# Kernel optimization log

Measured on AMD Instinct MI355X. Metric: run time of the kernel, lower is better.

The kernel has to match this reference:

```python
import jax, jax.numpy as jnp
import numpy as np
from jax import lax

EPS = 1e-06
S = 0.025
ALPHA = 0.98
DELTA = 2.0
R = 0.5


def setup_inputs() -> dict:
    key = jax.random.key(0)
    # magnitude spectrogram: [batch, freq, time], nonnegative
    x = jax.random.uniform(key, (32, 256, 4096), dtype=jnp.float32)
    return {"x": x}


def reference(x):
    # x: [B, F, T]; EMA smoother runs over the time axis (last dim).
    # m_0 = s*x_0 ; m_t = (1-s)*m_{t-1} + s*x_t  (init carry 0 reproduces m_0 = s*x_0)
    xt = jnp.moveaxis(x, 2, 0)  # [T, B, F]

    def step(m, frame):
        m = (1.0 - S) * m + S * frame
        return m, m

    _, M = lax.scan(step, jnp.zeros_like(xt[0]), xt)  # [T, B, F]
    M = jnp.moveaxis(M, 0, 2)  # [B, F, T]
    # power-law compression fused elementwise
    return (x / (M + EPS) ** ALPHA + DELTA) ** R - DELTA ** R
```

## Files before the change

### kernel.cpp

```cpp
#include <hip/hip_runtime.h>


constexpr int T_LEN = 4096;
constexpr int CHUNK = 1024;
constexpr int WARM  = 256;

constexpr float EPSF = 1e-6f;
constexpr float SF   = 0.025f;
constexpr float A1F  = 0.975f;

constexpr double dA1   = 0.975;
constexpr double dA2   = dA1 * dA1;
constexpr double dA4   = dA2 * dA2;
constexpr double dA8   = dA4 * dA4;
constexpr double dA16  = dA8 * dA8;
constexpr double dA32  = dA16 * dA16;
constexpr double dA64  = dA32 * dA32;
constexpr double dA128 = dA64 * dA64;
constexpr double dA256 = dA128 * dA128;
constexpr double dA512 = dA256 * dA256;

__global__ __launch_bounds__(256, 8) void pcen_kernel(
    const float* __restrict__ x, float* __restrict__ out)
{
    const int tid  = threadIdx.x;
    const int lane = tid & 63;
    const int wave = tid >> 6;
    const long long rbase = (long long)blockIdx.x * T_LEN;
    const int cbase = wave * CHUNK;

    const float4* __restrict__ px   = (const float4*)(x + rbase);
    float4* __restrict__       pout = (float4*)(out + rbase);

    const int f0 = (cbase >> 2) + lane * 4;
    float4 v0 = px[f0 + 0];
    float4 v1 = px[f0 + 1];
    float4 v2 = px[f0 + 2];
    float4 v3 = px[f0 + 3];
    float4 wv = make_float4(0.f, 0.f, 0.f, 0.f);
    if (wave > 0)
        wv = px[((cbase - WARM) >> 2) + lane];

    float T = 0.f;
    if (wave > 0) {
        float Lw = SF * wv.x;
        Lw = fmaf(A1F, Lw, SF * wv.y);
        Lw = fmaf(A1F, Lw, SF * wv.z);
        Lw = fmaf(A1F, Lw, SF * wv.w);
        int e = 63 - lane;
        float f = 1.f;
        if (e & 1)  f *= (float)dA4;
        if (e & 2)  f *= (float)dA8;
        if (e & 4)  f *= (float)dA16;
        if (e & 8)  f *= (float)dA32;
        if (e & 16) f *= (float)dA64;
        if (e & 32) f *= (float)dA128;
        float vs = f * Lw;
        vs += __shfl_xor(vs, 1,  64);
        vs += __shfl_xor(vs, 2,  64);
        vs += __shfl_xor(vs, 4,  64);
        vs += __shfl_xor(vs, 8,  64);
        vs += __shfl_xor(vs, 16, 64);
        vs += __shfl_xor(vs, 32, 64);
        T = vs;
    }

    float xv[16] = { v0.x, v0.y, v0.z, v0.w,
                     v1.x, v1.y, v1.z, v1.w,
                     v2.x, v2.y, v2.z, v2.w,
                     v3.x, v3.y, v3.z, v3.w };
    float S = 0.f;
#pragma unroll
    for (int k = 0; k < 16; ++k) S = fmaf(A1F, S, SF * xv[k]);

    float P = S, t;
    t = __shfl_up(P, 1,  64); if (lane >= 1)  P = fmaf((float)dA16,  t, P);
    t = __shfl_up(P, 2,  64); if (lane >= 2)  P = fmaf((float)dA32,  t, P);
    t = __shfl_up(P, 4,  64); if (lane >= 4)  P = fmaf((float)dA64,  t, P);
    t = __shfl_up(P, 8,  64); if (lane >= 8)  P = fmaf((float)dA128, t, P);
    t = __shfl_up(P, 16, 64); if (lane >= 16) P = fmaf((float)dA256, t, P);
    t = __shfl_up(P, 32, 64); if (lane >= 32) P = fmaf((float)dA512, t, P);

    float carry = __shfl_up(P, 1, 64);
    if (lane == 0) carry = 0.f;
    {
        int e = lane;
        float f = 1.f;
        if (e & 1)  f *= (float)dA16;
        if (e & 2)  f *= (float)dA32;
        if (e & 4)  f *= (float)dA64;
        if (e & 8)  f *= (float)dA128;
        if (e & 16) f *= (float)dA256;
        if (e & 32) f *= (float)dA512;
        carry = fmaf(f, T, carry);
    }

    const float SQRT_D = 1.41421356237309515f;
    float m = carry;
#pragma unroll
    for (int g = 0; g < 4; ++g) {
        float4 r;
        float* rp = &r.x;
#pragma unroll
        for (int j = 0; j < 4; ++j) {
            float xx = xv[g * 4 + j];
            m = fmaf(A1F, m, SF * xx);
            float p = __builtin_amdgcn_exp2f(-0.98f * __builtin_amdgcn_logf(m + EPSF));
            rp[j] = __fsqrt_rn(fmaf(xx, p, 2.0f)) - SQRT_D;
        }
        pout[f0 + g] = r;
    }
}

extern "C" void kernel_launch(void* const* d_in, const int* in_sizes, int n_in,
                              void* d_out, int out_size, void* d_ws, size_t ws_size,
                              hipStream_t stream) {
    const float* x = (const float*)d_in[0];
    float* out = (float*)d_out;
    const int rows = in_sizes[0] / T_LEN;
    pcen_kernel<<<dim3(rows), dim3(256), 0, stream>>>(x, out);
}
```

Baseline: 236.6 us.

## Use persistent grid-stride blocks with next-row prefetch and nontemporal stores

Launches a fixed grid of 2048 blocks that loop over the 8192 rows, loading the next row's data into registers while computing the current one. Per-lane decay factors are hoisted out of the loop, and outputs are written with nontemporal stores. The aim is to hide load latency and cut launch/tail overhead in a memory-bound kernel. In exchange it uses more registers, drops the occupancy hint, and runs fewer blocks, which could reduce memory-level parallelism.

```diff
diff --git a/kernel.cpp b/kernel.cpp
--- a/kernel.cpp
+++ b/kernel.cpp
@@ -4,10 +4,13 @@
 constexpr int T_LEN = 4096;
 constexpr int CHUNK = 1024;
 constexpr int WARM  = 256;
+constexpr int NBLK  = 2048;
 
 constexpr float EPSF = 1e-6f;
 constexpr float SF   = 0.025f;
 constexpr float A1F  = 0.975f;
+
+typedef float vfloat4 __attribute__((ext_vector_type(4)));
 
 constexpr double dA1   = 0.975;
 constexpr double dA2   = dA1 * dA1;
@@ -20,95 +23,120 @@
 constexpr double dA256 = dA128 * dA128;
 constexpr double dA512 = dA256 * dA256;
 
-__global__ __launch_bounds__(256, 8) void pcen_kernel(
-    const float* __restrict__ x, float* __restrict__ out)
+__global__ __launch_bounds__(256) void pcen_kernel(
+    const float* __restrict__ x, float* __restrict__ out, int rows)
 {
     const int tid  = threadIdx.x;
     const int lane = tid & 63;
     const int wave = tid >> 6;
-    const long long rbase = (long long)blockIdx.x * T_LEN;
     const int cbase = wave * CHUNK;
+    const int f0 = (cbase >> 2) + lane * 4;
+    const int fw = ((cbase - WARM) >> 2) + lane;
+    const int RQ = T_LEN / 4;
 
-    const float4* __restrict__ px   = (const float4*)(x + rbase);
-    float4* __restrict__       pout = (float4*)(out + rbase);
+    const vfloat4* __restrict__ px = (const vfloat4*)x;
 
-    const int f0 = (cbase >> 2) + lane * 4;
-    float4 v0 = px[f0 + 0];
-    float4 v1 = px[f0 + 1];
-    float4 v2 = px[f0 + 2];
-    float4 v3 = px[f0 + 3];
-    float4 wv = make_float4(0.f, 0.f, 0.f, 0.f);
-    if (wave > 0)
-        wv = px[((cbase - WARM) >> 2) + lane];
-
-    float T = 0.f;
-    if (wave > 0) {
-        float Lw = SF * wv.x;
-        Lw = fmaf(A1F, Lw, SF * wv.y);
-        Lw = fmaf(A1F, Lw, SF * wv.z);
-        Lw = fmaf(A1F, Lw, SF * wv.w);
+    float fwarm = 1.f;
+    {
         int e = 63 - lane;
-        float f = 1.f;
-        if (e & 1)  f *= (float)dA4;
-        if (e & 2)  f *= (float)dA8;
-        if (e & 4)  f *= (float)dA16;
-        if (e & 8)  f *= (float)dA32;
-        if (e & 16) f *= (float)dA64;
-        if (e & 32) f *= (float)dA128;
-        float vs = f * Lw;
-        vs += __shfl_xor(vs, 1,  64);
-        vs += __shfl_xor(vs, 2,  64);
-        vs += __shfl_xor(vs, 4,  64);
-        vs += __shfl_xor(vs, 8,  64);
-        vs += __shfl_xor(vs, 16, 64);
-        vs += __shfl_xor(vs, 32, 64);
-        T = vs;
+        if (e & 1)  fwarm *= (float)dA4;
+        if (e & 2)  fwarm *= (float)dA8;
+        if (e & 4)  fwarm *= (float)dA16;
+        if (e & 8)  fwarm *= (float)dA32;
+        if (e & 16) fwarm *= (float)dA64;
+        if (e & 32) fwarm *= (float)dA128;
+    }
+    float fcarry = 1.f;
+    {
+        int e = lane;
+        if (e & 1)  fcarry *= (float)dA16;
+        if (e & 2)  fcarry *= (float)dA32;
+        if (e & 4)  fcarry *= (float)dA64;
+        if (e & 8)  fcarry *= (float)dA128;
+        if (e & 16) fcarry *= (float)dA256;
+        if (e & 32) fcarry *= (float)dA512;
     }
 
-    float xv[16] = { v0.x, v0.y, v0.z, v0.w,
-                     v1.x, v1.y, v1.z, v1.w,
-                     v2.x, v2.y, v2.z, v2.w,
-                     v3.x, v3.y, v3.z, v3.w };
-    float S = 0.f;
-#pragma unroll
-    for (int k = 0; k < 16; ++k) S = fmaf(A1F, S, SF * xv[k]);
+    const vfloat4 zero4 = {0.f, 0.f, 0.f, 0.f};
 
-    float P = S, t;
-    t = __shfl_up(P, 1,  64); if (lane >= 1)  P = fmaf((float)dA16,  t, P);
-    t = __shfl_up(P, 2,  64); if (lane >= 2)  P = fmaf((float)dA32,  t, P);
-    t = __shfl_up(P, 4,  64); if (lane >= 4)  P = fmaf((float)dA64,  t, P);
-    t = __shfl_up(P, 8,  64); if (lane >= 8)  P = fmaf((float)dA128, t, P);
-    t = __shfl_up(P, 16, 64); if (lane >= 16) P = fmaf((float)dA256, t, P);
-    t = __shfl_up(P, 32, 64); if (lane >= 32) P = fmaf((float)dA512, t, P);
-
-    float carry = __shfl_up(P, 1, 64);
-    if (lane == 0) carry = 0.f;
-    {
-        int e = lane;
-        float f = 1.f;
-        if (e & 1)  f *= (float)dA16;
-        if (e & 2)  f *= (float)dA32;
-        if (e & 4)  f *= (float)dA64;
-        if (e & 8)  f *= (float)dA128;
-        if (e & 16) f *= (float)dA256;
-        if (e & 32) f *= (float)dA512;
-        carry = fmaf(f, T, carry);
+    int r = blockIdx.x;
+    vfloat4 v0 = zero4, v1 = zero4, v2 = zero4, v3 = zero4, wv = zero4;
+    if (r < rows) {
+        long long rb = (long long)r * RQ;
+        v0 = px[rb + f0 + 0];
+        v1 = px[rb + f0 + 1];
+        v2 = px[rb + f0 + 2];
+        v3 = px[rb + f0 + 3];
+        if (wave > 0) wv = px[rb + fw];
     }
 
     const float SQRT_D = 1.41421356237309515f;
-    float m = carry;
+
+    while (r < rows) {
+        const int rn = r + NBLK;
+        vfloat4 n0 = zero4, n1 = zero4, n2 = zero4, n3 = zero4, nw = zero4;
+        if (rn < rows) {
+            long long rbn = (long long)rn * RQ;
+            n0 = px[rbn + f0 + 0];
+            n1 = px[rbn + f0 + 1];
+            n2 = px[rbn + f0 + 2];
+            n3 = px[rbn + f0 + 3];
+            if (wave > 0) nw = px[rbn + fw];
+        }
+
+        float T = 0.f;
+        if (wave > 0) {
+            float Lw = SF * wv.x;
+            Lw = fmaf(A1F, Lw, SF * wv.y);
+            Lw = fmaf(A1F, Lw, SF * wv.z);
+            Lw = fmaf(A1F, Lw, SF * wv.w);
+            float vs = fwarm * Lw;
+            vs += __shfl_xor(vs, 1,  64);
+            vs += __shfl_xor(vs, 2,  64);
+            vs += __shfl_xor(vs, 4,  64);
+            vs += __shfl_xor(vs, 8,  64);
+            vs += __shfl_xor(vs, 16, 64);
+            vs += __shfl_xor(vs, 32, 64);
+            T = vs;
+        }
+
+        float xv[16] = { v0.x, v0.y, v0.z, v0.w,
+                         v1.x, v1.y, v1.z, v1.w,
+                         v2.x, v2.y, v2.z, v2.w,
+                         v3.x, v3.y, v3.z, v3.w };
+        float S = 0.f;
 #pragma unroll
-    for (int g = 0; g < 4; ++g) {
-        float4 r;
-        float* rp = &r.x;
+        for (int k = 0; k < 16; ++k) S = fmaf(A1F, S, SF * xv[k]);
+
+        float P = S, t;
+        t = __shfl_up(P, 1,  64); if (lane >= 1)  P = fmaf((float)dA16,  t, P);
+        t = __shfl_up(P, 2,  64); if (lane >= 2)  P = fmaf((float)dA32,  t, P);
+        t = __shfl_up(P, 4,  64); if (lane >= 4)  P = fmaf((float)dA64,  t, P);
+        t = __shfl_up(P, 8,  64); if (lane >= 8)  P = fmaf((float)dA128, t, P);
+        t = __shfl_up(P, 16, 64); if (lane >= 16) P = fmaf((float)dA256, t, P);
+        t = __shfl_up(P, 32, 64); if (lane >= 32) P = fmaf((float)dA512, t, P);
+
+        float carry = __shfl_up(P, 1, 64);
+        if (lane == 0) carry = 0.f;
+        carry = fmaf(fcarry, T, carry);
+
+        vfloat4* pout = (vfloat4*)out + (long long)r * RQ;
+        float m = carry;
 #pragma unroll
-        for (int j = 0; j < 4; ++j) {
-            float xx = xv[g * 4 + j];
-            m = fmaf(A1F, m, SF * xx);
-            float p = __builtin_amdgcn_exp2f(-0.98f * __builtin_amdgcn_logf(m + EPSF));
-            rp[j] = __fsqrt_rn(fmaf(xx, p, 2.0f)) - SQRT_D;
+        for (int g = 0; g < 4; ++g) {
+            vfloat4 rr;
+#pragma unroll
+            for (int j = 0; j < 4; ++j) {
+                float xx = xv[g * 4 + j];
+                m = fmaf(A1F, m, SF * xx);
+                float p = __builtin_amdgcn_exp2f(-0.98f * __builtin_amdgcn_logf(m + EPSF));
+                rr[j] = __fsqrt_rn(fmaf(xx, p, 2.0f)) - SQRT_D;
+            }
+            __builtin_nontemporal_store(rr, pout + f0 + g);
         }
-        pout[f0 + g] = r;
+
+        v0 = n0; v1 = n1; v2 = n2; v3 = n3; wv = nw;
+        r = rn;
     }
 }
 
@@ -118,5 +146,5 @@
     const float* x = (const float*)d_in[0];
     float* out = (float*)d_out;
     const int rows = in_sizes[0] / T_LEN;
-    pcen_kernel<<<dim3(rows), dim3(256), 0, stream>>>(x, out);
+    pcen_kernel<<<dim3(NBLK), dim3(256), 0, stream>>>(x, out, rows);
 }
```

New measurement: 367.1 us. 55.1% more time.
